# Kernel tuning notes

Hardware: AMD Instinct MI355X
Metric: run time of the kernel (lower is better)

The kernel has to match this reference:

```python
import jax, jax.numpy as jnp
import numpy as np

MARGIN = 1.0
EPS = 1e-05
B = 8192
D = 128
NUM_CLASSES = 256


def setup_inputs() -> dict:
    key = jax.random.key(0)
    k1, k2 = jax.random.split(key)
    feature = jax.random.normal(k1, (B, D), dtype=jnp.float32)
    label = jax.random.randint(k2, (B,), 0, NUM_CLASSES, dtype=jnp.int32)
    return {"feature": feature, "label": label}


def reference(feature, label):
    # Pairwise Euclidean distance matrix: ||x_i||^2 + ||x_j||^2 - 2 x_i.x_j + eps, then sqrt
    sq = jnp.sum(feature * feature, axis=1, keepdims=True)  # [B, 1]
    dist = jnp.sqrt(jnp.maximum(sq + sq.T - 2.0 * (feature @ feature.T) + EPS, 0.0))  # [B, B]

    same = label[:, None] == label[None, :]  # [B, B] bool, includes self on diagonal
    inf = jnp.array(jnp.inf, dtype=dist.dtype)

    # Original sorts each row and takes same[1]: the SECOND smallest same-label distance
    # (the smallest is the anchor itself, distance sqrt(eps)).
    d_same = jnp.where(same, dist, inf)
    two_smallest = -jax.lax.top_k(-d_same, 2)[0]  # [B, 2], ascending smallest two
    pos = two_smallest[:, 1]  # nearest positive excluding self

    # diff.min(): hardest (closest) negative per row
    neg = jnp.min(jnp.where(same, inf, dist), axis=1)

    hinge = jnp.maximum(MARGIN + pos - neg, 0.0)
    return jnp.mean(hinge)
```

## Files before the change

kernel.cpp:

```cpp
#include <hip/hip_runtime.h>
#include <math.h>


#define BN 8192
#define MARGIN_F 1.0f
#define EPS_F 1e-5f

typedef __attribute__((ext_vector_type(8))) short short8;
typedef __attribute__((ext_vector_type(4))) float floatx4;

__device__ __forceinline__ unsigned short bf16_rne(float x, float& r) {
    unsigned u = __float_as_uint(x);
    u += 0x7FFF + ((u >> 16) & 1);
    unsigned short h = (unsigned short)(u >> 16);
    r = __uint_as_float(((unsigned)h) << 16);
    return h;
}

__global__ __launch_bounds__(256) void prep_kernel(const float* __restrict__ f,
                                                   const int* __restrict__ lbl,
                                                   short8* __restrict__ fbT,
                                                   float2* __restrict__ lsq,
                                                   float* __restrict__ g_acc,
                                                   unsigned* __restrict__ counter) {
    int gid = blockIdx.x * 256 + threadIdx.x;
    if (gid == 0) { *g_acc = 0.f; *counter = 0u; }
    int row = gid >> 3, part = gid & 7;
    const float4* f4 = (const float4*)f + (size_t)row * 32 + part * 4;
    float s = 0.f;
#pragma unroll
    for (int cc = 0; cc < 2; ++cc) {
        float4 v0 = f4[cc * 2], v1 = f4[cc * 2 + 1];
        float r0, r1, r2, r3, r4, r5, r6, r7;
        short8 o;
        o[0] = (short)bf16_rne(v0.x, r0);
        o[1] = (short)bf16_rne(v0.y, r1);
        o[2] = (short)bf16_rne(v0.z, r2);
        o[3] = (short)bf16_rne(v0.w, r3);
        o[4] = (short)bf16_rne(v1.x, r4);
        o[5] = (short)bf16_rne(v1.y, r5);
        o[6] = (short)bf16_rne(v1.z, r6);
        o[7] = (short)bf16_rne(v1.w, r7);
        fbT[(size_t)(part * 2 + cc) * BN + row] = o;
        s += r0 * r0 + r1 * r1 + r2 * r2 + r3 * r3 +
             r4 * r4 + r5 * r5 + r6 * r6 + r7 * r7;
    }
    s += __shfl_xor(s, 1, 8);
    s += __shfl_xor(s, 2, 8);
    s += __shfl_xor(s, 4, 8);
    if (part == 0) {
        float2 p;
        p.x = s;
        p.y = __int_as_float(lbl[row]);
        lsq[row] = p;
    }
}

__global__ __launch_bounds__(256, 4) void work_kernel(const short8* __restrict__ fbT,
                                                      const int* __restrict__ lbl,
                                                      const float2* __restrict__ lsq,
                                                      float* __restrict__ part,
                                                      float* __restrict__ pos_d2) {
    const int t = threadIdx.x;
    const int lane = t & 63;
    const int wv = t >> 6;
    const int q = lane >> 4, c = lane & 15;
    const int bid = blockIdx.x;

    if (bid >= 1024) {
        __shared__ int midx[256];
        __shared__ int cnt;
        const int cls = bid - 1024;
        if (t == 0) cnt = 0;
        __syncthreads();
        for (int r = t; r < BN; r += 256) {
            if (lbl[r] == cls) {
                int p = atomicAdd(&cnt, 1);
                if (p < 256) midx[p] = r;
            }
        }
        __syncthreads();
        int n = cnt < 256 ? cnt : 256;
        if (n == 0) return;
        if (t < 256 && t >= n) midx[t] = midx[0];
        __syncthreads();

        const int ng = (n + 15) >> 4;
        for (int ig = wv; ig < ng; ig += 4) {
            short8 a[4];
            int arow = midx[ig * 16 + c];
#pragma unroll
            for (int ks = 0; ks < 4; ++ks)
                a[ks] = fbT[(size_t)(ks * 4 + q) * BN + arow];
            float s1[4], s2[4];
#pragma unroll
            for (int rg = 0; rg < 4; ++rg) { s1[rg] = INFINITY; s2[rg] = INFINITY; }

            for (int s = 0; s < ng; ++s) {
                int jslot = s * 16 + c;
                int jrow = midx[jslot];
                short8 b[4];
#pragma unroll
                for (int ks = 0; ks < 4; ++ks)
                    b[ks] = fbT[(size_t)(ks * 4 + q) * BN + jrow];
                float sj = lsq[jrow].x;
                bool valid = (jslot < n);

                floatx4 acc = (floatx4)0.f;
#pragma unroll
                for (int ks = 0; ks < 4; ++ks)
                    acc = __builtin_amdgcn_mfma_f32_16x16x32_bf16(a[ks], b[ks], acc, 0, 0, 0);
#pragma unroll
                for (int rg = 0; rg < 4; ++rg) {
                    float v = fmaf(-2.0f, acc[rg], sj);
                    float vs = valid ? v : INFINITY;
                    s2[rg] = fminf(s2[rg], fmaxf(s1[rg], vs));
                    s1[rg] = fminf(s1[rg], vs);
                }
            }
#pragma unroll
            for (int m = 1; m < 16; m <<= 1) {
#pragma unroll
                for (int rg = 0; rg < 4; ++rg) {
                    float o1 = __shfl_xor(s1[rg], m, 16);
                    float o2 = __shfl_xor(s2[rg], m, 16);
                    float lo = fminf(s1[rg], o1);
                    float hi = fminf(fmaxf(s1[rg], o1), fminf(s2[rg], o2));
                    s1[rg] = lo; s2[rg] = hi;
                }
            }
            if (c == 0) {
#pragma unroll
                for (int rg = 0; rg < 4; ++rg) {
                    int islot = ig * 16 + q * 4 + rg;
                    if (islot < n) {
                        int row = midx[islot];
                        pos_d2[row] = lsq[row].x + s2[rg];
                    }
                }
            }
        }
        return;
    }

    const int i0 = (bid & 63) * 128 + wv * 32;
    const int g = bid >> 6;
    const int jb = g * 512;

    short8 a[2][4];
#pragma unroll
    for (int mf = 0; mf < 2; ++mf) {
        int row = i0 + mf * 16 + c;
#pragma unroll
        for (int ks = 0; ks < 4; ++ks)
            a[mf][ks] = fbT[(size_t)(ks * 4 + q) * BN + row];
    }
    int li[2][4];
#pragma unroll
    for (int mf = 0; mf < 2; ++mf)
#pragma unroll
        for (int rg = 0; rg < 4; ++rg)
            li[mf][rg] = __float_as_int(lsq[i0 + mf * 16 + q * 4 + rg].y);

    float n1[2][4];
#pragma unroll
    for (int mf = 0; mf < 2; ++mf)
#pragma unroll
        for (int rg = 0; rg < 4; ++rg) n1[mf][rg] = INFINITY;

#pragma unroll 2
    for (int jt = 0; jt < 8; ++jt) {
        const int j0 = jb + jt * 64;

        int ljv[4]; float sjv[4];
#pragma unroll
        for (int nf = 0; nf < 4; ++nf) {
            float2 p = lsq[j0 + nf * 16 + c];
            sjv[nf] = p.x;
            ljv[nf] = __float_as_int(p.y);
        }

        floatx4 acc[2][4];
#pragma unroll
        for (int mf = 0; mf < 2; ++mf)
#pragma unroll
            for (int nf = 0; nf < 4; ++nf) acc[mf][nf] = (floatx4)0.f;

#pragma unroll
        for (int ks = 0; ks < 4; ++ks) {
            short8 b[4];
#pragma unroll
            for (int nf = 0; nf < 4; ++nf)
                b[nf] = fbT[(size_t)(ks * 4 + q) * BN + j0 + nf * 16 + c];
#pragma unroll
            for (int mf = 0; mf < 2; ++mf)
#pragma unroll
                for (int nf = 0; nf < 4; ++nf)
                    acc[mf][nf] = __builtin_amdgcn_mfma_f32_16x16x32_bf16(
                        a[mf][ks], b[nf], acc[mf][nf], 0, 0, 0);
        }

#pragma unroll
        for (int nf = 0; nf < 4; ++nf) {
#pragma unroll
            for (int mf = 0; mf < 2; ++mf)
#pragma unroll
                for (int rg = 0; rg < 4; ++rg) {
                    float v = fmaf(-2.0f, acc[mf][nf][rg], sjv[nf]);
                    float vd = (li[mf][rg] == ljv[nf]) ? INFINITY : v;
                    n1[mf][rg] = fminf(n1[mf][rg], vd);
                }
        }
    }

#pragma unroll
    for (int m = 1; m < 16; m <<= 1) {
#pragma unroll
        for (int mf = 0; mf < 2; ++mf)
#pragma unroll
            for (int rg = 0; rg < 4; ++rg)
                n1[mf][rg] = fminf(n1[mf][rg], __shfl_xor(n1[mf][rg], m, 16));
    }
    if (c == 0) {
#pragma unroll
        for (int mf = 0; mf < 2; ++mf)
#pragma unroll
            for (int rg = 0; rg < 4; ++rg)
                part[g * BN + i0 + mf * 16 + q * 4 + rg] = n1[mf][rg];
    }
}

__global__ __launch_bounds__(128) void merge_kernel(const float* __restrict__ part,
                                                    const float2* __restrict__ lsq,
                                                    const float* __restrict__ pos_d2,
                                                    float* __restrict__ g_acc,
                                                    unsigned* __restrict__ counter,
                                                    float* __restrict__ out) {
    int r = blockIdx.x * 128 + threadIdx.x;
    float n = INFINITY;
#pragma unroll
    for (int k = 0; k < 16; ++k) n = fminf(n, part[k * BN + r]);
    float si = lsq[r].x;
    float pos = sqrtf(fmaxf(pos_d2[r] + EPS_F, 0.f));
    float neg = sqrtf(fmaxf(si + n + EPS_F, 0.f));
    float h = fmaxf(MARGIN_F + pos - neg, 0.f);
    __shared__ float red[2];
#pragma unroll
    for (int m = 32; m >= 1; m >>= 1) h += __shfl_down(h, m, 64);
    if ((threadIdx.x & 63) == 0) red[threadIdx.x >> 6] = h;
    __syncthreads();
    if (threadIdx.x == 0) {
        atomicAdd(g_acc, red[0] + red[1]);
        __threadfence();
        unsigned old = atomicAdd(counter, 1u);
        if (old == 63u) {
            float tot = atomicAdd(g_acc, 0.0f);
            out[0] = tot / (float)BN;
        }
    }
}

extern "C" void kernel_launch(void* const* d_in, const int* in_sizes, int n_in,
                              void* d_out, int out_size, void* d_ws, size_t ws_size,
                              hipStream_t stream) {
    const float* f = (const float*)d_in[0];
    const int* lbl = (const int*)d_in[1];
    char* ws = (char*)d_ws;
    float2* lsq = (float2*)ws;
    short8* fbT = (short8*)(ws + 65536);
    float* part = (float*)(ws + 65536 + 2097152);
    float* pos_d2 = (float*)(ws + 65536 + 2097152 + 524288);
    float* g_acc = (float*)(ws + 65536 + 2097152 + 524288 + 32768);
    unsigned* counter = (unsigned*)(g_acc + 1);
    float* out = (float*)d_out;

    prep_kernel<<<256, 256, 0, stream>>>(f, lbl, fbT, lsq, g_acc, counter);
    work_kernel<<<1280, 256, 0, stream>>>(fbT, lbl, lsq, part, pos_d2);
    merge_kernel<<<64, 128, 0, stream>>>(part, lsq, pos_d2, g_acc, counter, out);
}
```

Measured before the change: 93.58 us.

## Fuse merge into work kernel via last-block reduction and halve column splits

```diff
diff --git a/kernel.cpp b/kernel.cpp
--- a/kernel.cpp
+++ b/kernel.cpp
@@ -21,10 +21,9 @@
                                                    const int* __restrict__ lbl,
                                                    short8* __restrict__ fbT,
                                                    float2* __restrict__ lsq,
-                                                   float* __restrict__ g_acc,
                                                    unsigned* __restrict__ counter) {
     int gid = blockIdx.x * 256 + threadIdx.x;
-    if (gid == 0) { *g_acc = 0.f; *counter = 0u; }
+    if (gid == 0) { *counter = 0u; }
     int row = gid >> 3, part = gid & 7;
     const float4* f4 = (const float4*)f + (size_t)row * 32 + part * 4;
     float s = 0.f;
@@ -56,21 +55,25 @@
     }
 }
 
-__global__ __launch_bounds__(256, 4) void work_kernel(const short8* __restrict__ fbT,
+__global__ __launch_bounds__(256, 3) void work_kernel(const short8* __restrict__ fbT,
                                                       const int* __restrict__ lbl,
                                                       const float2* __restrict__ lsq,
                                                       float* __restrict__ part,
-                                                      float* __restrict__ pos_d2) {
+                                                      float* __restrict__ pos_d2,
+                                                      unsigned* __restrict__ counter,
+                                                      float* __restrict__ out) {
     const int t = threadIdx.x;
     const int lane = t & 63;
     const int wv = t >> 6;
     const int q = lane >> 4, c = lane & 15;
     const int bid = blockIdx.x;
-
-    if (bid >= 1024) {
+    __shared__ unsigned s_rank;
+    __shared__ float red[4];
+
+    if (bid >= 512) {
         __shared__ int midx[256];
         __shared__ int cnt;
-        const int cls = bid - 1024;
+        const int cls = bid - 512;
         if (t == 0) cnt = 0;
         __syncthreads();
         for (int r = t; r < BN; r += 256) {
@@ -81,182 +84,174 @@
         }
         __syncthreads();
         int n = cnt < 256 ? cnt : 256;
-        if (n == 0) return;
-        if (t < 256 && t >= n) midx[t] = midx[0];
+        if (n > 0) {
+            if (t < 256 && t >= n) midx[t] = midx[0];
+            __syncthreads();
+
+            const int ng = (n + 15) >> 4;
+            for (int ig = wv; ig < ng; ig += 4) {
+                short8 a[4];
+                int arow = midx[ig * 16 + c];
+#pragma unroll
+                for (int ks = 0; ks < 4; ++ks)
+                    a[ks] = fbT[(size_t)(ks * 4 + q) * BN + arow];
+                float s1[4], s2[4];
+#pragma unroll
+                for (int rg = 0; rg < 4; ++rg) { s1[rg] = INFINITY; s2[rg] = INFINITY; }
+
+                for (int s = 0; s < ng; ++s) {
+                    int jslot = s * 16 + c;
+                    int jrow = midx[jslot];
+                    short8 b[4];
+#pragma unroll
+                    for (int ks = 0; ks < 4; ++ks)
+                        b[ks] = fbT[(size_t)(ks * 4 + q) * BN + jrow];
+                    float sj = lsq[jrow].x;
+                    bool valid = (jslot < n);
+
+                    floatx4 acc = (floatx4)0.f;
+#pragma unroll
+                    for (int ks = 0; ks < 4; ++ks)
+                        acc = __builtin_amdgcn_mfma_f32_16x16x32_bf16(a[ks], b[ks], acc, 0, 0, 0);
+#pragma unroll
+                    for (int rg = 0; rg < 4; ++rg) {
+                        float v = fmaf(-2.0f, acc[rg], sj);
+                        float vs = valid ? v : INFINITY;
+                        s2[rg] = fminf(s2[rg], fmaxf(s1[rg], vs));
+                        s1[rg] = fminf(s1[rg], vs);
+                    }
+                }
+#pragma unroll
+                for (int m = 1; m < 16; m <<= 1) {
+#pragma unroll
+                    for (int rg = 0; rg < 4; ++rg) {
+                        float o1 = __shfl_xor(s1[rg], m, 16);
+                        float o2 = __shfl_xor(s2[rg], m, 16);
+                        float lo = fminf(s1[rg], o1);
+                        float hi = fminf(fmaxf(s1[rg], o1), fminf(s2[rg], o2));
+                        s1[rg] = lo; s2[rg] = hi;
+                    }
+                }
+                if (c == 0) {
+#pragma unroll
+                    for (int rg = 0; rg < 4; ++rg) {
+                        int islot = ig * 16 + q * 4 + rg;
+                        if (islot < n) {
+                            int row = midx[islot];
+                            pos_d2[row] = lsq[row].x + s2[rg];
+                        }
+                    }
+                }
+            }
+        }
+    } else {
+        const int i0 = (bid & 63) * 128 + wv * 32;
+        const int g = bid >> 6;
+        const int jb = g * 1024;
+
+        short8 a[2][4];
+#pragma unroll
+        for (int mf = 0; mf < 2; ++mf) {
+            int row = i0 + mf * 16 + c;
+#pragma unroll
+            for (int ks = 0; ks < 4; ++ks)
+                a[mf][ks] = fbT[(size_t)(ks * 4 + q) * BN + row];
+        }
+        int li[2][4];
+#pragma unroll
+        for (int mf = 0; mf < 2; ++mf)
+#pragma unroll
+            for (int rg = 0; rg < 4; ++rg)
+                li[mf][rg] = __float_as_int(lsq[i0 + mf * 16 + q * 4 + rg].y);
+
+        float n1[2][4];
+#pragma unroll
+        for (int mf = 0; mf < 2; ++mf)
+#pragma unroll
+            for (int rg = 0; rg < 4; ++rg) n1[mf][rg] = INFINITY;
+
+#pragma unroll 2
+        for (int jt = 0; jt < 16; ++jt) {
+            const int j0 = jb + jt * 64;
+
+            int ljv[4]; float sjv[4];
+#pragma unroll
+            for (int nf = 0; nf < 4; ++nf) {
+                float2 p = lsq[j0 + nf * 16 + c];
+                sjv[nf] = p.x;
+                ljv[nf] = __float_as_int(p.y);
+            }
+
+            floatx4 acc[2][4];
+#pragma unroll
+            for (int mf = 0; mf < 2; ++mf)
+#pragma unroll
+                for (int nf = 0; nf < 4; ++nf) acc[mf][nf] = (floatx4)0.f;
+
+#pragma unroll
+            for (int ks = 0; ks < 4; ++ks) {
+                short8 b[4];
+#pragma unroll
+                for (int nf = 0; nf < 4; ++nf)
+                    b[nf] = fbT[(size_t)(ks * 4 + q) * BN + j0 + nf * 16 + c];
+#pragma unroll
+                for (int mf = 0; mf < 2; ++mf)
+#pragma unroll
+                    for (int nf = 0; nf < 4; ++nf)
+                        acc[mf][nf] = __builtin_amdgcn_mfma_f32_16x16x32_bf16(
+                            a[mf][ks], b[nf], acc[mf][nf], 0, 0, 0);
+            }
+
+#pragma unroll
+            for (int nf = 0; nf < 4; ++nf) {
+#pragma unroll
+                for (int mf = 0; mf < 2; ++mf)
+#pragma unroll
+                    for (int rg = 0; rg < 4; ++rg) {
+                        float v = fmaf(-2.0f, acc[mf][nf][rg], sjv[nf]);
+                        float vd = (li[mf][rg] == ljv[nf]) ? INFINITY : v;
+                        n1[mf][rg] = fminf(n1[mf][rg], vd);
+                    }
+            }
+        }
+
+#pragma unroll
+        for (int m = 1; m < 16; m <<= 1) {
+#pragma unroll
+            for (int mf = 0; mf < 2; ++mf)
+#pragma unroll
+                for (int rg = 0; rg < 4; ++rg)
+                    n1[mf][rg] = fminf(n1[mf][rg], __shfl_xor(n1[mf][rg], m, 16));
+        }
+        if (c == 0) {
+#pragma unroll
+            for (int mf = 0; mf < 2; ++mf)
+#pragma unroll
+                for (int rg = 0; rg < 4; ++rg)
+                    part[g * BN + i0 + mf * 16 + q * 4 + rg] = n1[mf][rg];
+        }
+    }
+
+    __threadfence();
+    if (t == 0) s_rank = atomicAdd(counter, 1u);
+    __syncthreads();
+    if (s_rank == 767u) {
+        __threadfence();
+        float sum = 0.f;
+        for (int it = 0; it < 32; ++it) {
+            int r = it * 256 + t;
+            float n = INFINITY;
+#pragma unroll
+            for (int k = 0; k < 8; ++k) n = fminf(n, part[k * BN + r]);
+            float pos = sqrtf(fmaxf(pos_d2[r] + EPS_F, 0.f));
+            float neg = sqrtf(fmaxf(lsq[r].x + n + EPS_F, 0.f));
+            sum += fmaxf(MARGIN_F + pos - neg, 0.f);
+        }
+#pragma unroll
+        for (int m = 32; m >= 1; m >>= 1) sum += __shfl_down(sum, m, 64);
+        if (lane == 0) red[wv] = sum;
         __syncthreads();
-
-        const int ng = (n + 15) >> 4;
-        for (int ig = wv; ig < ng; ig += 4) {
-            short8 a[4];
-            int arow = midx[ig * 16 + c];
-#pragma unroll
-            for (int ks = 0; ks < 4; ++ks)
-                a[ks] = fbT[(size_t)(ks * 4 + q) * BN + arow];
-            float s1[4], s2[4];
-#pragma unroll
-            for (int rg = 0; rg < 4; ++rg) { s1[rg] = INFINITY; s2[rg] = INFINITY; }
-
-            for (int s = 0; s < ng; ++s) {
-                int jslot = s * 16 + c;
-                int jrow = midx[jslot];
-                short8 b[4];
-#pragma unroll
-                for (int ks = 0; ks < 4; ++ks)
-                    b[ks] = fbT[(size_t)(ks * 4 + q) * BN + jrow];
-                float sj = lsq[jrow].x;
-                bool valid = (jslot < n);
-
-                floatx4 acc = (floatx4)0.f;
-#pragma unroll
-                for (int ks = 0; ks < 4; ++ks)
-                    acc = __builtin_amdgcn_mfma_f32_16x16x32_bf16(a[ks], b[ks], acc, 0, 0, 0);
-#pragma unroll
-                for (int rg = 0; rg < 4; ++rg) {
-                    float v = fmaf(-2.0f, acc[rg], sj);
-                    float vs = valid ? v : INFINITY;
-                    s2[rg] = fminf(s2[rg], fmaxf(s1[rg], vs));
-                    s1[rg] = fminf(s1[rg], vs);
-                }
-            }
-#pragma unroll
-            for (int m = 1; m < 16; m <<= 1) {
-#pragma unroll
-                for (int rg = 0; rg < 4; ++rg) {
-                    float o1 = __shfl_xor(s1[rg], m, 16);
-                    float o2 = __shfl_xor(s2[rg], m, 16);
-                    float lo = fminf(s1[rg], o1);
-                    float hi = fminf(fmaxf(s1[rg], o1), fminf(s2[rg], o2));
-                    s1[rg] = lo; s2[rg] = hi;
-                }
-            }
-            if (c == 0) {
-#pragma unroll
-                for (int rg = 0; rg < 4; ++rg) {
-                    int islot = ig * 16 + q * 4 + rg;
-                    if (islot < n) {
-                        int row = midx[islot];
-                        pos_d2[row] = lsq[row].x + s2[rg];
-                    }
-                }
-            }
-        }
-        return;
-    }
-
-    const int i0 = (bid & 63) * 128 + wv * 32;
-    const int g = bid >> 6;
-    const int jb = g * 512;
-
-    short8 a[2][4];
-#pragma unroll
-    for (int mf = 0; mf < 2; ++mf) {
-        int row = i0 + mf * 16 + c;
-#pragma unroll
-        for (int ks = 0; ks < 4; ++ks)
-            a[mf][ks] = fbT[(size_t)(ks * 4 + q) * BN + row];
-    }
-    int li[2][4];
-#pragma unroll
-    for (int mf = 0; mf < 2; ++mf)
-#pragma unroll
-        for (int rg = 0; rg < 4; ++rg)
-            li[mf][rg] = __float_as_int(lsq[i0 + mf * 16 + q * 4 + rg].y);
-
-    float n1[2][4];
-#pragma unroll
-    for (int mf = 0; mf < 2; ++mf)
-#pragma unroll
-        for (int rg = 0; rg < 4; ++rg) n1[mf][rg] = INFINITY;
-
-#pragma unroll 2
-    for (int jt = 0; jt < 8; ++jt) {
-        const int j0 = jb + jt * 64;
-
-        int ljv[4]; float sjv[4];
-#pragma unroll
-        for (int nf = 0; nf < 4; ++nf) {
-            float2 p = lsq[j0 + nf * 16 + c];
-            sjv[nf] = p.x;
-            ljv[nf] = __float_as_int(p.y);
-        }
-
-        floatx4 acc[2][4];
-#pragma unroll
-        for (int mf = 0; mf < 2; ++mf)
-#pragma unroll
-            for (int nf = 0; nf < 4; ++nf) acc[mf][nf] = (floatx4)0.f;
-
-#pragma unroll
-        for (int ks = 0; ks < 4; ++ks) {
-            short8 b[4];
-#pragma unroll
-            for (int nf = 0; nf < 4; ++nf)
-                b[nf] = fbT[(size_t)(ks * 4 + q) * BN + j0 + nf * 16 + c];
-#pragma unroll
-            for (int mf = 0; mf < 2; ++mf)
-#pragma unroll
-                for (int nf = 0; nf < 4; ++nf)
-                    acc[mf][nf] = __builtin_amdgcn_mfma_f32_16x16x32_bf16(
-                        a[mf][ks], b[nf], acc[mf][nf], 0, 0, 0);
-        }
-
-#pragma unroll
-        for (int nf = 0; nf < 4; ++nf) {
-#pragma unroll
-            for (int mf = 0; mf < 2; ++mf)
-#pragma unroll
-                for (int rg = 0; rg < 4; ++rg) {
-                    float v = fmaf(-2.0f, acc[mf][nf][rg], sjv[nf]);
-                    float vd = (li[mf][rg] == ljv[nf]) ? INFINITY : v;
-                    n1[mf][rg] = fminf(n1[mf][rg], vd);
-                }
-        }
-    }
-
-#pragma unroll
-    for (int m = 1; m < 16; m <<= 1) {
-#pragma unroll
-        for (int mf = 0; mf < 2; ++mf)
-#pragma unroll
-            for (int rg = 0; rg < 4; ++rg)
-                n1[mf][rg] = fminf(n1[mf][rg], __shfl_xor(n1[mf][rg], m, 16));
-    }
-    if (c == 0) {
-#pragma unroll
-        for (int mf = 0; mf < 2; ++mf)
-#pragma unroll
-            for (int rg = 0; rg < 4; ++rg)
-                part[g * BN + i0 + mf * 16 + q * 4 + rg] = n1[mf][rg];
-    }
-}
-
-__global__ __launch_bounds__(128) void merge_kernel(const float* __restrict__ part,
-                                                    const float2* __restrict__ lsq,
-                                                    const float* __restrict__ pos_d2,
-                                                    float* __restrict__ g_acc,
-                                                    unsigned* __restrict__ counter,
-                                                    float* __restrict__ out) {
-    int r = blockIdx.x * 128 + threadIdx.x;
-    float n = INFINITY;
-#pragma unroll
-    for (int k = 0; k < 16; ++k) n = fminf(n, part[k * BN + r]);
-    float si = lsq[r].x;
-    float pos = sqrtf(fmaxf(pos_d2[r] + EPS_F, 0.f));
-    float neg = sqrtf(fmaxf(si + n + EPS_F, 0.f));
-    float h = fmaxf(MARGIN_F + pos - neg, 0.f);
-    __shared__ float red[2];
-#pragma unroll
-    for (int m = 32; m >= 1; m >>= 1) h += __shfl_down(h, m, 64);
-    if ((threadIdx.x & 63) == 0) red[threadIdx.x >> 6] = h;
-    __syncthreads();
-    if (threadIdx.x == 0) {
-        atomicAdd(g_acc, red[0] + red[1]);
-        __threadfence();
-        unsigned old = atomicAdd(counter, 1u);
-        if (old == 63u) {
-            float tot = atomicAdd(g_acc, 0.0f);
-            out[0] = tot / (float)BN;
-        }
+        if (t == 0) out[0] = (red[0] + red[1] + red[2] + red[3]) / (float)BN;
     }
 }
 
@@ -269,12 +264,10 @@
     float2* lsq = (float2*)ws;
     short8* fbT = (short8*)(ws + 65536);
     float* part = (float*)(ws + 65536 + 2097152);
-    float* pos_d2 = (float*)(ws + 65536 + 2097152 + 524288);
-    float* g_acc = (float*)(ws + 65536 + 2097152 + 524288 + 32768);
-    unsigned* counter = (unsigned*)(g_acc + 1);
+    float* pos_d2 = (float*)(ws + 65536 + 2097152 + 262144);
+    unsigned* counter = (unsigned*)(ws + 65536 + 2097152 + 262144 + 32768);
     float* out = (float*)d_out;
 
-    prep_kernel<<<256, 256, 0, stream>>>(f, lbl, fbT, lsq, g_acc, counter);
-    work_kernel<<<1280, 256, 0, stream>>>(fbT, lbl, lsq, part, pos_d2);
-    merge_kernel<<<64, 128, 0, stream>>>(part, lsq, pos_d2, g_acc, counter, out);
-}
+    prep_kernel<<<256, 256, 0, stream>>>(f, lbl, fbT, lsq, counter);
+    work_kernel<<<768, 256, 0, stream>>>(fbT, lbl, lsq, part, pos_d2, counter, out);
+}
```

Result: slower. 152.8 us (+63.3%).
